# Performance work log

Measured on AMD Instinct MI355X. Metric: run time of the kernel, lower is better.

Reference implementation:

```python
import jax, jax.numpy as jnp
import numpy as np

T, B, D, H, L = 64, 512, 1536, 1024, 4
DISCOUNT = 0.997
LAM = 0.95


def setup_inputs() -> dict:
    key = jax.random.key(0)
    ks = jax.random.split(key, 3 + L + 1)
    inp = {
        'feat': jax.random.normal(ks[0], (T, B, D), dtype=jnp.float32),
        'reward': jax.random.normal(ks[1], (T - 1, B), dtype=jnp.float32),
        'cont': jnp.ones((T, B), dtype=jnp.float32),
    }
    scale = 0.02
    dims = [D] + [H] * L
    for i in range(L):
        inp[f'W{i}'] = jax.random.normal(ks[3 + i], (dims[i], dims[i + 1]), dtype=jnp.float32) * scale
        inp[f'b{i}'] = jnp.zeros((dims[i + 1],), dtype=jnp.float32)
    inp['Wo'] = jax.random.normal(ks[3 + L], (H,), dtype=jnp.float32) * scale
    inp['bo'] = jnp.zeros((), dtype=jnp.float32)
    return inp


def reference(feat, reward, cont, W0, b0, W1, b1, W2, b2, W3, b3, Wo, bo):
    # Value-net MLP (mean of critic dist): [T, B, D] -> [T, B]
    h = feat
    for W, b in ((W0, b0), (W1, b1), (W2, b2), (W3, b3)):
        h = jax.nn.silu(h @ W + b)
    value = h @ Wo + bo  # [T, B]

    disc = cont[1:] * DISCOUNT                      # [T-1, B]
    deltas = reward + disc * value[1:] - value[:-1]  # [T-1, B]

    # GAE: adv_t = delta_t + disc_t * lambda * adv_{t+1}, adv_T = 0
    def step(adv_next, xs):
        delta, dl = xs
        adv = delta + dl * adv_next
        return adv, adv

    _, advs = jax.lax.scan(step, jnp.zeros_like(value[0]),
                           (deltas, disc * LAM), reverse=True)
    ret = advs + value[:-1]   # lambda-return target, [T-1, B]
    baseline = value[:-1]
    return ret, baseline
```

## Files before the change

kernel.cpp:

```cpp
#include <hip/hip_runtime.h>
#include <hip/hip_bf16.h>

#define T_DIM 64
#define B_DIM 512
#define D_DIM 1536
#define H_DIM 1024
#define M_DIM (T_DIM * B_DIM)
#define DISCOUNT 0.997f
#define LAM 0.95f

#define BM 128
#define BN 256
#define BK 64
#define TILES_M 256
#define TILES_N 4
#define N_XCD 8

typedef __bf16 bf16x8 __attribute__((ext_vector_type(8)));
typedef float  f32x4  __attribute__((ext_vector_type(4)));

__device__ __forceinline__ void async_load16(const void* g, void* l) {
    __builtin_amdgcn_global_load_lds(
        (const __attribute__((address_space(1))) void*)g,
        (__attribute__((address_space(3))) void*)l,
        16, 0, 0);
}

__device__ __forceinline__ unsigned short f2bf_raw(float f) {
    __hip_bfloat16 h = __float2bfloat16(f);
    return *reinterpret_cast<unsigned short*>(&h);
}

__global__ __launch_bounds__(256) void cvt_bf16_kernel(
    const float* __restrict__ x, __hip_bfloat16* __restrict__ y, long n4) {
    long i = (long)blockIdx.x * blockDim.x + threadIdx.x;
    if (i >= n4) return;
    float4 v = reinterpret_cast<const float4*>(x)[i];
    ushort4 o;
    o.x = f2bf_raw(v.x);
    o.y = f2bf_raw(v.y);
    o.z = f2bf_raw(v.z);
    o.w = f2bf_raw(v.w);
    reinterpret_cast<ushort4*>(y)[i] = o;
}

__global__ __launch_bounds__(256) void transpose_cvt_all_kernel(
    const float* __restrict__ W0, const float* __restrict__ W1,
    const float* __restrict__ W2, const float* __restrict__ W3,
    __hip_bfloat16* __restrict__ T0, __hip_bfloat16* __restrict__ T1,
    __hip_bfloat16* __restrict__ T2, __hip_bfloat16* __restrict__ T3) {
    __shared__ float tile[32][33];
    int z = blockIdx.z;
    const float* W;
    __hip_bfloat16* Tt;
    int K;
    if (z == 0)      { W = W0; Tt = T0; K = D_DIM; }
    else if (z == 1) { W = W1; Tt = T1; K = H_DIM; }
    else if (z == 2) { W = W2; Tt = T2; K = H_DIM; }
    else             { W = W3; Tt = T3; K = H_DIM; }
    int k0 = blockIdx.x * 32, n0 = blockIdx.y * 32;
    if (k0 >= K) return;
    int tx = threadIdx.x, ty = threadIdx.y;
    #pragma unroll
    for (int r = ty; r < 32; r += 8)
        tile[r][tx] = W[(size_t)(k0 + r) * H_DIM + n0 + tx];
    __syncthreads();
    #pragma unroll
    for (int r = ty; r < 32; r += 8)
        Tt[(size_t)(n0 + r) * K + k0 + tx] = __float2bfloat16(tile[tx][r]);
}

__global__ __launch_bounds__(512, 4) void gemm_silu_kernel(
    const __hip_bfloat16* __restrict__ A,
    const __hip_bfloat16* __restrict__ Bt,
    const float* __restrict__ bias,
    __hip_bfloat16* __restrict__ C,
    int K) {

    __shared__ alignas(16) __hip_bfloat16 As[BM * BK];
    __shared__ alignas(16) __hip_bfloat16 Bs[BN * BK];

    const int tid  = threadIdx.x;
    const int wave = tid >> 6;
    const int lane = tid & 63;
    const int sub  = lane >> 3;
    const int quad = lane >> 4;
    const int r16  = lane & 15;
    const int wm   = wave & 1;
    const int wn   = wave >> 1;

    const int l     = blockIdx.x;
    const int xcd   = l & (N_XCD - 1);
    const int local = l >> 3;
    const int tn    = local & (TILES_N - 1);
    const int tm    = (xcd << 5) | (local >> 2);
    const int m0 = tm * BM;
    const int n0 = tn * BN;

    const int scol = (((lane & 7) ^ sub) << 3);

    const __hip_bfloat16* ga[2];
    const __hip_bfloat16* gb[4];
    #pragma unroll
    for (int i = 0; i < 2; ++i)
        ga[i] = A + (size_t)(m0 + (wave * 2 + i) * 8 + sub) * K + scol;
    #pragma unroll
    for (int i = 0; i < 4; ++i)
        gb[i] = Bt + (size_t)(n0 + (wave * 4 + i) * 8 + sub) * K + scol;

    f32x4 acc[4][4];
    #pragma unroll
    for (int i = 0; i < 4; ++i)
        #pragma unroll
        for (int j = 0; j < 4; ++j)
            acc[i][j] = (f32x4){0.f, 0.f, 0.f, 0.f};

    for (int k0 = 0; k0 < K; k0 += BK) {
        #pragma unroll
        for (int i = 0; i < 2; ++i) {
            async_load16(ga[i], &As[(wave * 2 + i) * 512]);
            ga[i] += BK;
        }
        #pragma unroll
        for (int i = 0; i < 4; ++i) {
            async_load16(gb[i], &Bs[(wave * 4 + i) * 512]);
            gb[i] += BK;
        }
        __syncthreads();

        #pragma unroll
        for (int kk = 0; kk < BK; kk += 32) {
            bf16x8 af[4], bf[4];
            #pragma unroll
            for (int i = 0; i < 4; ++i) {
                int m_l = wm * 64 + i * 16 + r16;
                int sa  = ((kk >> 3) + quad) ^ (m_l & 7);
                af[i] = *reinterpret_cast<const bf16x8*>(&As[m_l * BK + sa * 8]);
                int n_l = wn * 64 + i * 16 + r16;
                int sb  = ((kk >> 3) + quad) ^ (n_l & 7);
                bf[i] = *reinterpret_cast<const bf16x8*>(&Bs[n_l * BK + sb * 8]);
            }
            #pragma unroll
            for (int i = 0; i < 4; ++i)
                #pragma unroll
                for (int j = 0; j < 4; ++j)
                    acc[i][j] = __builtin_amdgcn_mfma_f32_16x16x32_bf16(
                        af[i], bf[j], acc[i][j], 0, 0, 0);
        }
        __syncthreads();
    }

    #pragma unroll
    for (int j = 0; j < 4; ++j) {
        int col = n0 + wn * 64 + j * 16 + r16;
        float bj = bias[col];
        #pragma unroll
        for (int i = 0; i < 4; ++i) {
            int row_base = m0 + wm * 64 + i * 16 + quad * 4;
            #pragma unroll
            for (int rr = 0; rr < 4; ++rr) {
                float v = acc[i][j][rr] + bj;
                float s = v / (1.f + __expf(-v));
                C[(size_t)(row_base + rr) * H_DIM + col] = __float2bfloat16(s);
            }
        }
    }
}

__global__ __launch_bounds__(256) void gemv_value_kernel(
    const __hip_bfloat16* __restrict__ H,
    const float* __restrict__ Wo,
    const float* __restrict__ bo_p,
    float* __restrict__ value, int M) {
    int wave = threadIdx.x >> 6, lane = threadIdx.x & 63;
    int row = blockIdx.x * 4 + wave;
    if (row >= M) return;
    const __hip_bfloat16* hrow = H + (size_t)row * H_DIM;
    float sum = 0.f;
    #pragma unroll
    for (int half = 0; half < 2; ++half) {
        int col = half * 512 + lane * 8;
        uint4 raw = *reinterpret_cast<const uint4*>(hrow + col);
        const __hip_bfloat16* hp = reinterpret_cast<const __hip_bfloat16*>(&raw);
        #pragma unroll
        for (int e = 0; e < 8; ++e)
            sum += __bfloat162float(hp[e]) * Wo[col + e];
    }
    #pragma unroll
    for (int off = 32; off > 0; off >>= 1)
        sum += __shfl_down(sum, off, 64);
    if (lane == 0) value[row] = sum + bo_p[0];
}

__global__ __launch_bounds__(64) void gae_kernel(
    const float* __restrict__ value,
    const float* __restrict__ reward,
    const float* __restrict__ cont,
    float* __restrict__ out) {
    int b = blockIdx.x * blockDim.x + threadIdx.x;
    if (b >= B_DIM) return;
    float adv = 0.f;
    float v_next = value[(T_DIM - 1) * B_DIM + b];
    for (int t = T_DIM - 2; t >= 0; --t) {
        float v_t  = value[t * B_DIM + b];
        float disc = cont[(t + 1) * B_DIM + b] * DISCOUNT;
        float delta = reward[t * B_DIM + b] + disc * v_next - v_t;
        adv = delta + disc * LAM * adv;
        out[t * B_DIM + b] = adv + v_t;
        out[(T_DIM - 1) * B_DIM + t * B_DIM + b] = v_t;
        v_next = v_t;
    }
}

extern "C" void kernel_launch(void* const* d_in, const int* in_sizes, int n_in,
                              void* d_out, int out_size, void* d_ws, size_t ws_size,
                              hipStream_t stream) {
    const float* feat   = (const float*)d_in[0];
    const float* reward = (const float*)d_in[1];
    const float* cont   = (const float*)d_in[2];
    const float* W[4]   = {(const float*)d_in[3], (const float*)d_in[5],
                           (const float*)d_in[7], (const float*)d_in[9]};
    const float* bias[4] = {(const float*)d_in[4], (const float*)d_in[6],
                            (const float*)d_in[8], (const float*)d_in[10]};
    const float* Wo = (const float*)d_in[11];
    const float* bo = (const float*)d_in[12];
    float* out = (float*)d_out;

    char* ws = (char*)d_ws;
    __hip_bfloat16* Xb = (__hip_bfloat16*)ws; ws += (size_t)M_DIM * D_DIM * 2;
    __hip_bfloat16* Ha = (__hip_bfloat16*)ws; ws += (size_t)M_DIM * H_DIM * 2;
    __hip_bfloat16* Hb = (__hip_bfloat16*)ws; ws += (size_t)M_DIM * H_DIM * 2;
    __hip_bfloat16* Wt0 = (__hip_bfloat16*)ws; ws += (size_t)H_DIM * D_DIM * 2;
    __hip_bfloat16* Wt1 = (__hip_bfloat16*)ws; ws += (size_t)H_DIM * H_DIM * 2;
    __hip_bfloat16* Wt2 = (__hip_bfloat16*)ws; ws += (size_t)H_DIM * H_DIM * 2;
    __hip_bfloat16* Wt3 = (__hip_bfloat16*)ws; ws += (size_t)H_DIM * H_DIM * 2;
    float* value = (float*)ws; ws += (size_t)M_DIM * 4;

    long n4 = (long)M_DIM * D_DIM / 4;
    cvt_bf16_kernel<<<(int)((n4 + 255) / 256), 256, 0, stream>>>(feat, Xb, n4);

    transpose_cvt_all_kernel<<<dim3(D_DIM / 32, H_DIM / 32, 4), dim3(32, 8), 0, stream>>>(
        W[0], W[1], W[2], W[3], Wt0, Wt1, Wt2, Wt3);

    const int nblocks = TILES_M * TILES_N;
    gemm_silu_kernel<<<nblocks, 512, 0, stream>>>(Xb, Wt0, bias[0], Ha, D_DIM);
    gemm_silu_kernel<<<nblocks, 512, 0, stream>>>(Ha, Wt1, bias[1], Hb, H_DIM);
    gemm_silu_kernel<<<nblocks, 512, 0, stream>>>(Hb, Wt2, bias[2], Ha, H_DIM);
    gemm_silu_kernel<<<nblocks, 512, 0, stream>>>(Ha, Wt3, bias[3], Hb, H_DIM);

    gemv_value_kernel<<<M_DIM / 4, 256, 0, stream>>>(Hb, Wo, bo, value, M_DIM);

    gae_kernel<<<8, 64, 0, stream>>>(value, reward, cont, out);
}
```

Before: 677.5 us.

## Double-buffer LDS and enlarge GEMM tile to 256x256 with phased MFMA clusters

The GEMM block tile grows from 128x256 to 256x256, and LDS is double-buffered so global-to-LDS loads for the next K step overlap MFMA work on the current one. Each K step is split into four phases. Each phase interleaves a partial async stage, LDS fragment reads, barriers and an MFMA cluster run under raised wave priority. The aim is to hide global-load latency and raise arithmetic intensity per LDS byte, at the cost of more accumulator registers and occupancy lowered to 2 blocks per CU.

```diff
diff --git a/kernel.cpp b/kernel.cpp
--- a/kernel.cpp
+++ b/kernel.cpp
@@ -9,11 +9,11 @@
 #define DISCOUNT 0.997f
 #define LAM 0.95f
 
-#define BM 128
+#define BM 256
 #define BN 256
 #define BK 64
-#define TILES_M 256
-#define TILES_N 4
+#define TILES_M (M_DIM / BM)
+#define TILES_N (H_DIM / BN)
 #define N_XCD 8
 
 typedef __bf16 bf16x8 __attribute__((ext_vector_type(8)));
@@ -70,15 +70,19 @@
         Tt[(size_t)(n0 + r) * K + k0 + tx] = __float2bfloat16(tile[tx][r]);
 }
 
-__global__ __launch_bounds__(512, 4) void gemm_silu_kernel(
+__global__ __launch_bounds__(512, 2) void gemm_silu_kernel(
     const __hip_bfloat16* __restrict__ A,
     const __hip_bfloat16* __restrict__ Bt,
     const float* __restrict__ bias,
     __hip_bfloat16* __restrict__ C,
     int K) {
 
-    __shared__ alignas(16) __hip_bfloat16 As[BM * BK];
-    __shared__ alignas(16) __hip_bfloat16 Bs[BN * BK];
+    __shared__ alignas(16) __hip_bfloat16 lds[65536];
+
+    __hip_bfloat16* const A0 = lds;
+    __hip_bfloat16* const A1 = lds + 16384;
+    __hip_bfloat16* const B0 = lds + 32768;
+    __hip_bfloat16* const B1 = lds + 49152;
 
     const int tid  = threadIdx.x;
     const int wave = tid >> 6;
@@ -93,74 +97,139 @@
     const int xcd   = l & (N_XCD - 1);
     const int local = l >> 3;
     const int tn    = local & (TILES_N - 1);
-    const int tm    = (xcd << 5) | (local >> 2);
+    const int tm    = (xcd << 4) | (local >> 2);
     const int m0 = tm * BM;
     const int n0 = tn * BN;
 
-    const int scol = (((lane & 7) ^ sub) << 3);
-
-    const __hip_bfloat16* ga[2];
-    const __hip_bfloat16* gb[4];
-    #pragma unroll
-    for (int i = 0; i < 2; ++i)
-        ga[i] = A + (size_t)(m0 + (wave * 2 + i) * 8 + sub) * K + scol;
-    #pragma unroll
-    for (int i = 0; i < 4; ++i)
-        gb[i] = Bt + (size_t)(n0 + (wave * 4 + i) * 8 + sub) * K + scol;
-
-    f32x4 acc[4][4];
-    #pragma unroll
-    for (int i = 0; i < 4; ++i)
+    const int scol = ((lane & 7) ^ sub) << 3;
+
+    const __hip_bfloat16* aBase = A  + (size_t)(m0 + wave * 16 + sub) * K + scol;
+    const __hip_bfloat16* bBase = Bt + (size_t)(n0 + wave * 16 + sub) * K + scol;
+
+    f32x4 acc[8][4];
+    #pragma unroll
+    for (int i = 0; i < 8; ++i)
         #pragma unroll
         for (int j = 0; j < 4; ++j)
             acc[i][j] = (f32x4){0.f, 0.f, 0.f, 0.f};
 
-    for (int k0 = 0; k0 < K; k0 += BK) {
+    #pragma unroll
+    for (int p = 0; p < 2; ++p)
         #pragma unroll
         for (int i = 0; i < 2; ++i) {
-            async_load16(ga[i], &As[(wave * 2 + i) * 512]);
-            ga[i] += BK;
+            async_load16(aBase + (size_t)(p * 128 + i * 8) * K,
+                         A0 + (p * 16 + wave * 2 + i) * 512);
+            async_load16(bBase + (size_t)(p * 128 + i * 8) * K,
+                         B0 + (p * 16 + wave * 2 + i) * 512);
         }
+    __syncthreads();
+
+#define STAGE_A(p) do { \
+        async_load16(aBase + (size_t)((p) * 128    ) * K + kofs, \
+                     An + ((p) * 16 + wave * 2    ) * 512); \
+        async_load16(aBase + (size_t)((p) * 128 + 8) * K + kofs, \
+                     An + ((p) * 16 + wave * 2 + 1) * 512); \
+    } while (0)
+#define STAGE_B(p) do { \
+        async_load16(bBase + (size_t)((p) * 128    ) * K + kofs, \
+                     Bn + ((p) * 16 + wave * 2    ) * 512); \
+        async_load16(bBase + (size_t)((p) * 128 + 8) * K + kofs, \
+                     Bn + ((p) * 16 + wave * 2 + 1) * 512); \
+    } while (0)
+#define READ_A(mq) do { \
+        _Pragma("unroll") \
+        for (int ii = 0; ii < 4; ++ii) { \
+            const int m_l = wm * 128 + ((mq) * 4 + ii) * 16 + r16; \
+            _Pragma("unroll") \
+            for (int ks = 0; ks < 2; ++ks) \
+                af[ii][ks] = *reinterpret_cast<const bf16x8*>( \
+                    &Ac[m_l * BK + (((ks * 4 + quad) ^ (m_l & 7)) << 3)]); \
+        } \
+    } while (0)
+#define READ_B(nq) do { \
+        _Pragma("unroll") \
+        for (int jj = 0; jj < 2; ++jj) { \
+            const int n_l = wn * 64 + ((nq) * 2 + jj) * 16 + r16; \
+            _Pragma("unroll") \
+            for (int ks = 0; ks < 2; ++ks) \
+                bfr[jj][ks] = *reinterpret_cast<const bf16x8*>( \
+                    &Bc[n_l * BK + (((ks * 4 + quad) ^ (n_l & 7)) << 3)]); \
+        } \
+    } while (0)
+#define CLUSTER(mq, nq) do { \
+        __builtin_amdgcn_s_setprio(1); \
+        _Pragma("unroll") \
+        for (int ii = 0; ii < 4; ++ii) \
+            _Pragma("unroll") \
+            for (int jj = 0; jj < 2; ++jj) { \
+                acc[(mq)*4+ii][(nq)*2+jj] = __builtin_amdgcn_mfma_f32_16x16x32_bf16( \
+                    af[ii][0], bfr[jj][0], acc[(mq)*4+ii][(nq)*2+jj], 0, 0, 0); \
+                acc[(mq)*4+ii][(nq)*2+jj] = __builtin_amdgcn_mfma_f32_16x16x32_bf16( \
+                    af[ii][1], bfr[jj][1], acc[(mq)*4+ii][(nq)*2+jj], 0, 0, 0); \
+            } \
+        __builtin_amdgcn_s_setprio(0); \
+    } while (0)
+#define BAR() __builtin_amdgcn_s_barrier()
+
+    const int NT = K / BK;
+    for (int t = 0; t < NT; ++t) {
+        const bool last = (t == NT - 1);
+        const __hip_bfloat16* Ac = (t & 1) ? A1 : A0;
+        const __hip_bfloat16* Bc = (t & 1) ? B1 : B0;
+        __hip_bfloat16* An = (t & 1) ? A0 : A1;
+        __hip_bfloat16* Bn = (t & 1) ? B0 : B1;
+        const size_t kofs = (size_t)(t + 1) * BK;
+
+        bf16x8 af[4][2], bfr[2][2];
+
+        if (!last) STAGE_A(0);
+        READ_B(0);
+        READ_A(0);
+        BAR();
+        CLUSTER(0, 0);
+        BAR();
+
+        if (!last) STAGE_A(1);
+        READ_A(1);
+        BAR();
+        CLUSTER(1, 0);
+        BAR();
+
+        if (!last) STAGE_B(0);
+        READ_B(1);
+        BAR();
+        CLUSTER(1, 1);
+        BAR();
+
+        if (!last) STAGE_B(1);
+        READ_A(0);
+        BAR();
+        CLUSTER(0, 1);
+        if (!last) {
+            asm volatile("s_waitcnt vmcnt(0)" ::: "memory");
+            __builtin_amdgcn_sched_barrier(0);
+        }
+        BAR();
+    }
+
+#undef STAGE_A
+#undef STAGE_B
+#undef READ_A
+#undef READ_B
+#undef CLUSTER
+#undef BAR
+
+    #pragma unroll
+    for (int j = 0; j < 4; ++j) {
+        const int col = n0 + wn * 64 + j * 16 + r16;
+        const float bj = bias[col];
         #pragma unroll
-        for (int i = 0; i < 4; ++i) {
-            async_load16(gb[i], &Bs[(wave * 4 + i) * 512]);
-            gb[i] += BK;
-        }
-        __syncthreads();
-
-        #pragma unroll
-        for (int kk = 0; kk < BK; kk += 32) {
-            bf16x8 af[4], bf[4];
-            #pragma unroll
-            for (int i = 0; i < 4; ++i) {
-                int m_l = wm * 64 + i * 16 + r16;
-                int sa  = ((kk >> 3) + quad) ^ (m_l & 7);
-                af[i] = *reinterpret_cast<const bf16x8*>(&As[m_l * BK + sa * 8]);
-                int n_l = wn * 64 + i * 16 + r16;
-                int sb  = ((kk >> 3) + quad) ^ (n_l & 7);
-                bf[i] = *reinterpret_cast<const bf16x8*>(&Bs[n_l * BK + sb * 8]);
-            }
-            #pragma unroll
-            for (int i = 0; i < 4; ++i)
-                #pragma unroll
-                for (int j = 0; j < 4; ++j)
-                    acc[i][j] = __builtin_amdgcn_mfma_f32_16x16x32_bf16(
-                        af[i], bf[j], acc[i][j], 0, 0, 0);
-        }
-        __syncthreads();
-    }
-
-    #pragma unroll
-    for (int j = 0; j < 4; ++j) {
-        int col = n0 + wn * 64 + j * 16 + r16;
-        float bj = bias[col];
-        #pragma unroll
-        for (int i = 0; i < 4; ++i) {
-            int row_base = m0 + wm * 64 + i * 16 + quad * 4;
+        for (int i = 0; i < 8; ++i) {
+            const int row_base = m0 + wm * 128 + i * 16 + quad * 4;
             #pragma unroll
             for (int rr = 0; rr < 4; ++rr) {
-                float v = acc[i][j][rr] + bj;
-                float s = v / (1.f + __expf(-v));
+                const float v = acc[i][j][rr] + bj;
+                const float s = v / (1.f + __expf(-v));
                 C[(size_t)(row_base + rr) * H_DIM + col] = __float2bfloat16(s);
             }
         }
```

New measurement: 705.9 us. 4.2% more time.

## Enlarge GEMM tile to 256x256 with a 4-stage async LDS pipeline

Applied to the files above, without the earlier changes.

Rewrites the bf16 GEMM+SiLU main loop to use 256x256 output tiles with BK=32 and a four-buffer LDS ring. Global-to-LDS async loads are issued three stages ahead, so there is one barrier per iteration instead of two and memory latency overlaps with MFMA work. MFMA issue priority is raised during the compute phase. The larger tile raises arithmetic intensity per block, at the cost of more accumulator registers (occupancy lowered to 2 blocks per CU), 128KB of LDS, and half as many blocks in the grid.

```diff
diff --git a/kernel.cpp b/kernel.cpp
--- a/kernel.cpp
+++ b/kernel.cpp
@@ -9,11 +9,11 @@
 #define DISCOUNT 0.997f
 #define LAM 0.95f
 
-#define BM 128
+#define BM 256
 #define BN 256
-#define BK 64
-#define TILES_M 256
-#define TILES_N 4
+#define BK 32
+#define TILES_M (M_DIM / BM)
+#define TILES_N (H_DIM / BN)
 #define N_XCD 8
 
 typedef __bf16 bf16x8 __attribute__((ext_vector_type(8)));
@@ -70,20 +70,18 @@
         Tt[(size_t)(n0 + r) * K + k0 + tx] = __float2bfloat16(tile[tx][r]);
 }
 
-__global__ __launch_bounds__(512, 4) void gemm_silu_kernel(
+__global__ __launch_bounds__(512, 2) void gemm_silu_kernel(
     const __hip_bfloat16* __restrict__ A,
     const __hip_bfloat16* __restrict__ Bt,
     const float* __restrict__ bias,
     __hip_bfloat16* __restrict__ C,
     int K) {
 
-    __shared__ alignas(16) __hip_bfloat16 As[BM * BK];
-    __shared__ alignas(16) __hip_bfloat16 Bs[BN * BK];
+    __shared__ alignas(16) __hip_bfloat16 lds[65536];
 
     const int tid  = threadIdx.x;
     const int wave = tid >> 6;
     const int lane = tid & 63;
-    const int sub  = lane >> 3;
     const int quad = lane >> 4;
     const int r16  = lane & 15;
     const int wm   = wave & 1;
@@ -93,74 +91,87 @@
     const int xcd   = l & (N_XCD - 1);
     const int local = l >> 3;
     const int tn    = local & (TILES_N - 1);
-    const int tm    = (xcd << 5) | (local >> 2);
+    const int tm    = (xcd << 4) | (local >> 2);
     const int m0 = tm * BM;
     const int n0 = tn * BN;
 
-    const int scol = (((lane & 7) ^ sub) << 3);
-
-    const __hip_bfloat16* ga[2];
-    const __hip_bfloat16* gb[4];
-    #pragma unroll
-    for (int i = 0; i < 2; ++i)
-        ga[i] = A + (size_t)(m0 + (wave * 2 + i) * 8 + sub) * K + scol;
-    #pragma unroll
-    for (int i = 0; i < 4; ++i)
-        gb[i] = Bt + (size_t)(n0 + (wave * 4 + i) * 8 + sub) * K + scol;
-
-    f32x4 acc[4][4];
-    #pragma unroll
-    for (int i = 0; i < 4; ++i)
+    const int rsub = lane >> 2;
+    const int cgrp = lane & 3;
+    const int scol = ((cgrp ^ (rsub & 3)) << 3);
+    const __hip_bfloat16* gA = A  + (size_t)(m0 + wave * 32 + rsub) * K + scol;
+    const __hip_bfloat16* gB = Bt + (size_t)(n0 + wave * 32 + rsub) * K + scol;
+    const int ldsOf0 = (wave * 32) * 32;
+    const int ldsOf1 = (wave * 32 + 16) * 32;
+
+    const int swz    = ((quad ^ (r16 & 3)) << 3);
+    const int rdoffA = (wm * 128 + r16) * 32 + swz;
+    const int rdoffB = (wn * 64  + r16) * 32 + swz;
+
+    f32x4 acc[8][4];
+    #pragma unroll
+    for (int i = 0; i < 8; ++i)
         #pragma unroll
         for (int j = 0; j < 4; ++j)
             acc[i][j] = (f32x4){0.f, 0.f, 0.f, 0.f};
 
-    for (int k0 = 0; k0 < K; k0 += BK) {
+#define STAGE(tt) do { \
+        const int sbb = (tt) & 3; \
+        __hip_bfloat16* Ab_ = &lds[sbb * 8192]; \
+        __hip_bfloat16* Bb_ = &lds[32768 + sbb * 8192]; \
+        const size_t ko_ = (size_t)(tt) * BK; \
+        async_load16(gA + ko_,                 Ab_ + ldsOf0); \
+        async_load16(gA + ko_ + (size_t)16 * K, Ab_ + ldsOf1); \
+        async_load16(gB + ko_,                 Bb_ + ldsOf0); \
+        async_load16(gB + ko_ + (size_t)16 * K, Bb_ + ldsOf1); \
+    } while (0)
+
+#define BODY(t, VMCNT, DOSTAGE) do { \
+        asm volatile("s_waitcnt vmcnt(" #VMCNT ")" ::: "memory"); \
+        __builtin_amdgcn_s_barrier(); \
+        __builtin_amdgcn_sched_barrier(0); \
+        const int bb = (t) & 3; \
+        const __hip_bfloat16* Ab = &lds[bb * 8192]; \
+        const __hip_bfloat16* Bb = &lds[32768 + bb * 8192]; \
+        bf16x8 af[8], bfr[4]; \
+        _Pragma("unroll") \
+        for (int i = 0; i < 8; ++i) \
+            af[i] = *reinterpret_cast<const bf16x8*>(Ab + rdoffA + i * 512); \
+        _Pragma("unroll") \
+        for (int j = 0; j < 4; ++j) \
+            bfr[j] = *reinterpret_cast<const bf16x8*>(Bb + rdoffB + j * 512); \
+        if (DOSTAGE) STAGE((t) + 3); \
+        __builtin_amdgcn_s_setprio(1); \
+        _Pragma("unroll") \
+        for (int i = 0; i < 8; ++i) \
+            _Pragma("unroll") \
+            for (int j = 0; j < 4; ++j) \
+                acc[i][j] = __builtin_amdgcn_mfma_f32_16x16x32_bf16( \
+                    af[i], bfr[j], acc[i][j], 0, 0, 0); \
+        __builtin_amdgcn_s_setprio(0); \
+    } while (0)
+
+    STAGE(0); STAGE(1); STAGE(2);
+
+    const int NT = K / BK;
+    for (int t = 0; t < NT - 2; ++t)
+        BODY(t, 8, (t + 3 < NT));
+    BODY(NT - 2, 4, false);
+    BODY(NT - 1, 0, false);
+
+#undef STAGE
+#undef BODY
+
+    #pragma unroll
+    for (int j = 0; j < 4; ++j) {
+        const int col = n0 + wn * 64 + j * 16 + r16;
+        const float bj = bias[col];
         #pragma unroll
-        for (int i = 0; i < 2; ++i) {
-            async_load16(ga[i], &As[(wave * 2 + i) * 512]);
-            ga[i] += BK;
-        }
-        #pragma unroll
-        for (int i = 0; i < 4; ++i) {
-            async_load16(gb[i], &Bs[(wave * 4 + i) * 512]);
-            gb[i] += BK;
-        }
-        __syncthreads();
-
-        #pragma unroll
-        for (int kk = 0; kk < BK; kk += 32) {
-            bf16x8 af[4], bf[4];
-            #pragma unroll
-            for (int i = 0; i < 4; ++i) {
-                int m_l = wm * 64 + i * 16 + r16;
-                int sa  = ((kk >> 3) + quad) ^ (m_l & 7);
-                af[i] = *reinterpret_cast<const bf16x8*>(&As[m_l * BK + sa * 8]);
-                int n_l = wn * 64 + i * 16 + r16;
-                int sb  = ((kk >> 3) + quad) ^ (n_l & 7);
-                bf[i] = *reinterpret_cast<const bf16x8*>(&Bs[n_l * BK + sb * 8]);
-            }
-            #pragma unroll
-            for (int i = 0; i < 4; ++i)
-                #pragma unroll
-                for (int j = 0; j < 4; ++j)
-                    acc[i][j] = __builtin_amdgcn_mfma_f32_16x16x32_bf16(
-                        af[i], bf[j], acc[i][j], 0, 0, 0);
-        }
-        __syncthreads();
-    }
-
-    #pragma unroll
-    for (int j = 0; j < 4; ++j) {
-        int col = n0 + wn * 64 + j * 16 + r16;
-        float bj = bias[col];
-        #pragma unroll
-        for (int i = 0; i < 4; ++i) {
-            int row_base = m0 + wm * 64 + i * 16 + quad * 4;
+        for (int i = 0; i < 8; ++i) {
+            const int row_base = m0 + wm * 128 + i * 16 + quad * 4;
             #pragma unroll
             for (int rr = 0; rr < 4; ++rr) {
-                float v = acc[i][j][rr] + bj;
-                float s = v / (1.f + __expf(-v));
+                const float v = acc[i][j][rr] + bj;
+                const float s = v / (1.f + __expf(-v));
                 C[(size_t)(row_base + rr) * H_DIM + col] = __float2bfloat16(s);
             }
         }
```

New measurement: 717.9 us. 6.0% more time.

## Fuse value head GEMV into last GEMM epilogue and vectorize epilogue stores

Applied to the files above, without the earlier changes.

The last GEMM layer now folds the SiLU output into a dot product with Wo in its epilogue. Partial sums are reduced across lanes, through LDS, and with atomicAdd into a value buffer that is zeroed in the convert kernel. This removes the separate GEMV kernel and the write and re-read of the final hidden activation, and the bias bo is now added in the GAE kernel. Swapping the MFMA operands transposes the accumulator layout so the other layers can store four contiguous bf16 columns per row, giving wider stores. The cost is float atomic contention and order-dependent rounding in the value sums.

```diff
diff --git a/kernel.cpp b/kernel.cpp
--- a/kernel.cpp
+++ b/kernel.cpp
@@ -32,9 +32,12 @@
 }
 
 __global__ __launch_bounds__(256) void cvt_bf16_kernel(
-    const float* __restrict__ x, __hip_bfloat16* __restrict__ y, long n4) {
+    const float* __restrict__ x, __hip_bfloat16* __restrict__ y, long n4,
+    float* __restrict__ value) {
     long i = (long)blockIdx.x * blockDim.x + threadIdx.x;
     if (i >= n4) return;
+    if (i < M_DIM / 4)
+        reinterpret_cast<float4*>(value)[i] = (float4){0.f, 0.f, 0.f, 0.f};
     float4 v = reinterpret_cast<const float4*>(x)[i];
     ushort4 o;
     o.x = f2bf_raw(v.x);
@@ -75,7 +78,9 @@
     const __hip_bfloat16* __restrict__ Bt,
     const float* __restrict__ bias,
     __hip_bfloat16* __restrict__ C,
-    int K) {
+    int K,
+    const float* __restrict__ Wo,
+    float* __restrict__ value) {
 
     __shared__ alignas(16) __hip_bfloat16 As[BM * BK];
     __shared__ alignas(16) __hip_bfloat16 Bs[BN * BK];
@@ -145,64 +150,82 @@
                 #pragma unroll
                 for (int j = 0; j < 4; ++j)
                     acc[i][j] = __builtin_amdgcn_mfma_f32_16x16x32_bf16(
-                        af[i], bf[j], acc[i][j], 0, 0, 0);
+                        bf[j], af[i], acc[i][j], 0, 0, 0);
         }
         __syncthreads();
     }
 
-    #pragma unroll
-    for (int j = 0; j < 4; ++j) {
-        int col = n0 + wn * 64 + j * 16 + r16;
-        float bj = bias[col];
+    if (value == nullptr) {
+        #pragma unroll
+        for (int j = 0; j < 4; ++j) {
+            const int c0 = n0 + wn * 64 + j * 16 + quad * 4;
+            const float4 b4 = *reinterpret_cast<const float4*>(&bias[c0]);
+            const float* bp = reinterpret_cast<const float*>(&b4);
+            #pragma unroll
+            for (int i = 0; i < 4; ++i) {
+                const int row = m0 + wm * 64 + i * 16 + r16;
+                ushort4 o;
+                unsigned short* op = reinterpret_cast<unsigned short*>(&o);
+                #pragma unroll
+                for (int rr = 0; rr < 4; ++rr) {
+                    const float v = acc[i][j][rr] + bp[rr];
+                    const float s = v / (1.f + __expf(-v));
+                    op[rr] = f2bf_raw(s);
+                }
+                *reinterpret_cast<ushort4*>(&C[(size_t)row * H_DIM + c0]) = o;
+            }
+        }
+    } else {
+        float part[4];
+        #pragma unroll
+        for (int i = 0; i < 4; ++i) part[i] = 0.f;
+        #pragma unroll
+        for (int j = 0; j < 4; ++j) {
+            const int c0 = n0 + wn * 64 + j * 16 + quad * 4;
+            const float4 b4 = *reinterpret_cast<const float4*>(&bias[c0]);
+            const float4 w4 = *reinterpret_cast<const float4*>(&Wo[c0]);
+            const float* bp = reinterpret_cast<const float*>(&b4);
+            const float* wp = reinterpret_cast<const float*>(&w4);
+            #pragma unroll
+            for (int i = 0; i < 4; ++i) {
+                #pragma unroll
+                for (int rr = 0; rr < 4; ++rr) {
+                    const float v = acc[i][j][rr] + bp[rr];
+                    const float s = v / (1.f + __expf(-v));
+                    part[i] += s * wp[rr];
+                }
+            }
+        }
+        float* lds_v = reinterpret_cast<float*>(As);
         #pragma unroll
         for (int i = 0; i < 4; ++i) {
-            int row_base = m0 + wm * 64 + i * 16 + quad * 4;
-            #pragma unroll
-            for (int rr = 0; rr < 4; ++rr) {
-                float v = acc[i][j][rr] + bj;
-                float s = v / (1.f + __expf(-v));
-                C[(size_t)(row_base + rr) * H_DIM + col] = __float2bfloat16(s);
-            }
+            float p = part[i];
+            p += __shfl_xor(p, 16, 64);
+            p += __shfl_xor(p, 32, 64);
+            if (quad == 0)
+                lds_v[(wm * 64 + i * 16 + r16) * 4 + wn] = p;
+        }
+        __syncthreads();
+        if (tid < BM) {
+            const float* row = &lds_v[tid * 4];
+            atomicAdd(&value[m0 + tid], row[0] + row[1] + row[2] + row[3]);
         }
     }
-}
-
-__global__ __launch_bounds__(256) void gemv_value_kernel(
-    const __hip_bfloat16* __restrict__ H,
-    const float* __restrict__ Wo,
-    const float* __restrict__ bo_p,
-    float* __restrict__ value, int M) {
-    int wave = threadIdx.x >> 6, lane = threadIdx.x & 63;
-    int row = blockIdx.x * 4 + wave;
-    if (row >= M) return;
-    const __hip_bfloat16* hrow = H + (size_t)row * H_DIM;
-    float sum = 0.f;
-    #pragma unroll
-    for (int half = 0; half < 2; ++half) {
-        int col = half * 512 + lane * 8;
-        uint4 raw = *reinterpret_cast<const uint4*>(hrow + col);
-        const __hip_bfloat16* hp = reinterpret_cast<const __hip_bfloat16*>(&raw);
-        #pragma unroll
-        for (int e = 0; e < 8; ++e)
-            sum += __bfloat162float(hp[e]) * Wo[col + e];
-    }
-    #pragma unroll
-    for (int off = 32; off > 0; off >>= 1)
-        sum += __shfl_down(sum, off, 64);
-    if (lane == 0) value[row] = sum + bo_p[0];
 }
 
 __global__ __launch_bounds__(64) void gae_kernel(
     const float* __restrict__ value,
     const float* __restrict__ reward,
     const float* __restrict__ cont,
+    const float* __restrict__ bo_p,
     float* __restrict__ out) {
     int b = blockIdx.x * blockDim.x + threadIdx.x;
     if (b >= B_DIM) return;
+    const float bo = bo_p[0];
     float adv = 0.f;
-    float v_next = value[(T_DIM - 1) * B_DIM + b];
+    float v_next = value[(T_DIM - 1) * B_DIM + b] + bo;
     for (int t = T_DIM - 2; t >= 0; --t) {
-        float v_t  = value[t * B_DIM + b];
+        float v_t  = value[t * B_DIM + b] + bo;
         float disc = cont[(t + 1) * B_DIM + b] * DISCOUNT;
         float delta = reward[t * B_DIM + b] + disc * v_next - v_t;
         adv = delta + disc * LAM * adv;
@@ -237,18 +260,20 @@
     float* value = (float*)ws; ws += (size_t)M_DIM * 4;
 
     long n4 = (long)M_DIM * D_DIM / 4;
-    cvt_bf16_kernel<<<(int)((n4 + 255) / 256), 256, 0, stream>>>(feat, Xb, n4);
+    cvt_bf16_kernel<<<(int)((n4 + 255) / 256), 256, 0, stream>>>(feat, Xb, n4, value);
 
     transpose_cvt_all_kernel<<<dim3(D_DIM / 32, H_DIM / 32, 4), dim3(32, 8), 0, stream>>>(
         W[0], W[1], W[2], W[3], Wt0, Wt1, Wt2, Wt3);
 
     const int nblocks = TILES_M * TILES_N;
-    gemm_silu_kernel<<<nblocks, 512, 0, stream>>>(Xb, Wt0, bias[0], Ha, D_DIM);
-    gemm_silu_kernel<<<nblocks, 512, 0, stream>>>(Ha, Wt1, bias[1], Hb, H_DIM);
-    gemm_silu_kernel<<<nblocks, 512, 0, stream>>>(Hb, Wt2, bias[2], Ha, H_DIM);
-    gemm_silu_kernel<<<nblocks, 512, 0, stream>>>(Ha, Wt3, bias[3], Hb, H_DIM);
-
-    gemv_value_kernel<<<M_DIM / 4, 256, 0, stream>>>(Hb, Wo, bo, value, M_DIM);
-
-    gae_kernel<<<8, 64, 0, stream>>>(value, reward, cont, out);
-}
+    gemm_silu_kernel<<<nblocks, 512, 0, stream>>>(Xb, Wt0, bias[0], Ha, D_DIM,
+                                                  nullptr, nullptr);
+    gemm_silu_kernel<<<nblocks, 512, 0, stream>>>(Ha, Wt1, bias[1], Hb, H_DIM,
+                                                  nullptr, nullptr);
+    gemm_silu_kernel<<<nblocks, 512, 0, stream>>>(Hb, Wt2, bias[2], Ha, H_DIM,
+                                                  nullptr, nullptr);
+    gemm_silu_kernel<<<nblocks, 512, 0, stream>>>(Ha, Wt3, bias[3], Hb, H_DIM,
+                                                  Wo, value);
+
+    gae_kernel<<<8, 64, 0, stream>>>(value, reward, cont, bo, out);
+}
```

Result: no change. 673.8 us (-0.5%).
